# Performance work log

Hardware: AMD Instinct MI355X
Metric: run time of the kernel (lower is better)

Reference implementation:

```python
import jax, jax.numpy as jnp
import numpy as np

C = 512
B, H, W = 8, 64, 64
GROUPS = 32
EPS = 1e-6


def setup_inputs() -> dict:
    key = jax.random.key(0)
    ks = jax.random.split(key, 6)
    s = 1.0 / np.sqrt(C)
    return {
        "x": jax.random.normal(ks[0], (B, C, H, W), dtype=jnp.float32),
        "gn_scale": jnp.ones((C,), jnp.float32),
        "gn_bias": jnp.zeros((C,), jnp.float32),
        "wq": jax.random.normal(ks[1], (C, C), jnp.float32) * s,
        "bq": jnp.zeros((C,), jnp.float32),
        "wk": jax.random.normal(ks[2], (C, C), jnp.float32) * s,
        "bk": jnp.zeros((C,), jnp.float32),
        "wv": jax.random.normal(ks[3], (C, C), jnp.float32) * s,
        "bv": jnp.zeros((C,), jnp.float32),
        "wo": jax.random.normal(ks[4], (C, C), jnp.float32) * s,
        "bo": jnp.zeros((C,), jnp.float32),
    }


def group_norm(x, scale, bias):
    # x: [b, c, h, w]; GroupNorm(32 groups, eps=1e-6, affine)
    b, c, h, w = x.shape
    xg = x.reshape(b, GROUPS, c // GROUPS, h, w)
    mean = xg.mean(axis=(2, 3, 4), keepdims=True)
    var = xg.var(axis=(2, 3, 4), keepdims=True)
    xg = (xg - mean) * jax.lax.rsqrt(var + EPS)
    return xg.reshape(b, c, h, w) * scale[None, :, None, None] + bias[None, :, None, None]


def reference(x, gn_scale, gn_bias, wq, bq, wk, bk, wv, bv, wo, bo):
    b, c, h, w = x.shape
    n = h * w
    hn = group_norm(x, gn_scale, gn_bias).reshape(b, c, n)  # [b,c,n]
    # 1x1 convs == channel matmuls
    q = jnp.einsum('oc,bcn->bon', wq, hn) + bq[None, :, None]
    k = jnp.einsum('oc,bcn->bon', wk, hn) + bk[None, :, None]
    v = jnp.einsum('oc,bcn->bon', wv, hn) + bv[None, :, None]
    # scores: [b, n_query, n_key], softmax over keys
    scores = jnp.einsum('bcn,bcm->bnm', q, k) * (float(c) ** -0.5)
    attn = jax.nn.softmax(scores, axis=2)
    # out[b,c,i] = sum_j v[b,c,j] * attn[b,i,j]
    out = jnp.einsum('bcm,bnm->bcn', v, attn)
    out = jnp.einsum('oc,bcn->bon', wo, out) + bo[None, :, None]
    return x + out.reshape(b, c, h, w)
```

## Files before the change

### kernel.cpp

```cpp
#include <hip/hip_runtime.h>
#include <hip/hip_bf16.h>


typedef __bf16 bf16_t;
typedef __bf16 bf16x8 __attribute__((ext_vector_type(8)));
typedef __bf16 bf16x4 __attribute__((ext_vector_type(4)));
typedef float  f32x4  __attribute__((ext_vector_type(4)));

#define CDIM 512
#define NSP  4096
#define L2E  1.4426950408889634f

typedef __attribute__((address_space(1))) const void* as1_cvp;
typedef __attribute__((address_space(3))) void*       as3_vp;

__device__ __forceinline__ void gload_lds16(const void* g, void* l) {
  __builtin_amdgcn_global_load_lds((as1_cvp)g, (as3_vp)l, 16, 0, 0);
}

__global__ __launch_bounds__(256) void f32_to_bf16_k(const float* __restrict__ in,
                                                     bf16_t* __restrict__ out, int n) {
  int i = (blockIdx.x * 256 + threadIdx.x) * 4;
  if (i < n) {
    float4 v = *(const float4*)(in + i);
    bf16x4 o;
    o[0] = (bf16_t)v.x; o[1] = (bf16_t)v.y; o[2] = (bf16_t)v.z; o[3] = (bf16_t)v.w;
    *(bf16x4*)(out + i) = o;
  }
}

__global__ __launch_bounds__(256) void gn_stats_k(const float* __restrict__ x,
                                                  float* __restrict__ stats) {
  const int gid = blockIdx.x;
  const float4* base = (const float4*)(x + (long)gid * 65536);
  float s = 0.f, ss = 0.f;
  for (int i = threadIdx.x; i < 16384; i += 256) {
    float4 t = base[i];
    s  += t.x + t.y + t.z + t.w;
    ss += t.x*t.x + t.y*t.y + t.z*t.z + t.w*t.w;
  }
#pragma unroll
  for (int o = 32; o; o >>= 1) { s += __shfl_xor(s, o); ss += __shfl_xor(ss, o); }
  __shared__ float rs[4], rss[4];
  const int lane = threadIdx.x & 63, wid = threadIdx.x >> 6;
  if (lane == 0) { rs[wid] = s; rss[wid] = ss; }
  __syncthreads();
  if (threadIdx.x == 0) {
    s  = rs[0] + rs[1] + rs[2] + rs[3];
    ss = rss[0] + rss[1] + rss[2] + rss[3];
    float mean = s * (1.f / 65536.f);
    float var  = ss * (1.f / 65536.f) - mean * mean;
    stats[gid]       = mean;
    stats[256 + gid] = rsqrtf(var + 1e-6f);
  }
}

__global__ __launch_bounds__(256) void gn_apply_k(const float* __restrict__ x,
                                                  const float* __restrict__ stats,
                                                  const float* __restrict__ gw,
                                                  const float* __restrict__ gb,
                                                  bf16_t* __restrict__ hnT) {
  __shared__ float tile[64 * 65];
  const int n0 = blockIdx.x * 64;
  const int c0 = blockIdx.y * 64;
  const int b  = blockIdx.z;
  const int tid = threadIdx.x;
  {
    const int cl = tid >> 2, nq = tid & 3;
    const int c = c0 + cl;
    const int g = c >> 4;
    const float mean = stats[b * 32 + g];
    const float rstd = stats[256 + b * 32 + g];
    const float a  = rstd * gw[c];
    const float bb = gb[c] - mean * a;
    const float4* xr = (const float4*)(x + ((long)b * CDIM + c) * NSP + n0 + nq * 16);
#pragma unroll
    for (int i = 0; i < 4; i++) {
      float4 t = xr[i];
      float* d = &tile[cl * 65 + nq * 16 + i * 4];
      d[0] = t.x * a + bb; d[1] = t.y * a + bb; d[2] = t.z * a + bb; d[3] = t.w * a + bb;
    }
  }
  __syncthreads();
  {
    const int nl = tid >> 2, cq = tid & 3;
    union { bf16_t h[16]; uint4 v[2]; } o;
#pragma unroll
    for (int j = 0; j < 16; j++) o.h[j] = (bf16_t)tile[(cq * 16 + j) * 65 + nl];
    bf16_t* dst = hnT + ((long)b * NSP + n0 + nl) * CDIM + c0 + cq * 16;
    ((uint4*)dst)[0] = o.v[0];
    ((uint4*)dst)[1] = o.v[1];
  }
}

template <int MODE>
__global__ __launch_bounds__(256) void gemm_bt_k(
    const bf16_t* __restrict__ A, long sAb, long ldA,
    const bf16_t* __restrict__ B, long sBb, long ldB,
    void* __restrict__ Cout, long sCb, long ldC, void* __restrict__ Cout2,
    int M, int N, int K,
    const float* __restrict__ bias_row,
    const float* __restrict__ bias_col,
    float scale,
    const float* __restrict__ residual, long sRb) {
  __shared__ __align__(16) bf16_t sA[128 * 32];
  __shared__ __align__(16) bf16_t sB[128 * 32];

  const int tid  = threadIdx.x;
  const int lane = tid & 63;
  const int wid  = tid >> 6;
  const int wm = wid >> 1, wn = wid & 1;
  const int b = blockIdx.z;
  const int rowBase = blockIdx.y * 128;
  const int colBase = blockIdx.x * 128;

  const bf16_t* Ab = A + (long)b * sAb + (long)rowBase * ldA;
  const bf16_t* Bb = B + (long)b * sBb + (long)colBase * ldB;

  f32x4 acc[4][4];
#pragma unroll
  for (int i = 0; i < 4; i++)
#pragma unroll
    for (int j = 0; j < 4; j++) acc[i][j] = (f32x4){0.f, 0.f, 0.f, 0.f};

  const int q0 = tid, q1 = tid + 256;
  const int r0 = q0 >> 2, k0c = (q0 & 3) * 8;
  const int r1 = q1 >> 2, k1c = (q1 & 3) * 8;
  const int mrow  = lane & 15;
  const int kfrag = (lane >> 4) * 8;

  for (int kt = 0; kt < K; kt += 32) {
    gload_lds16(Ab + (long)r0 * ldA + kt + k0c, sA + q0 * 8);
    gload_lds16(Ab + (long)r1 * ldA + kt + k1c, sA + q1 * 8);
    gload_lds16(Bb + (long)r0 * ldB + kt + k0c, sB + q0 * 8);
    gload_lds16(Bb + (long)r1 * ldB + kt + k1c, sB + q1 * 8);
    __syncthreads();
    bf16x8 af[4], bfr[4];
#pragma unroll
    for (int t = 0; t < 4; t++) {
      af[t]  = *(const bf16x8*)&sA[(wm * 64 + t * 16 + mrow) * 32 + kfrag];
      bfr[t] = *(const bf16x8*)&sB[(wn * 64 + t * 16 + mrow) * 32 + kfrag];
    }
#pragma unroll
    for (int i = 0; i < 4; i++)
#pragma unroll
      for (int j = 0; j < 4; j++)
        acc[i][j] = __builtin_amdgcn_mfma_f32_16x16x32_bf16(af[i], bfr[j], acc[i][j], 0, 0, 0);
    __syncthreads();
  }

  const int quad = lane >> 4;
  const int colf = lane & 15;
#pragma unroll
  for (int i = 0; i < 4; i++) {
#pragma unroll
    for (int j = 0; j < 4; j++) {
#pragma unroll
      for (int r = 0; r < 4; r++) {
        const int row = rowBase + wm * 64 + i * 16 + quad * 4 + r;
        const int col = colBase + wn * 64 + j * 16 + colf;
        float v = acc[i][j][r];
        if (MODE == 2) {
          if (col < 512)
            ((bf16_t*)Cout)[(long)b * sCb + (long)row * ldC + col] =
                (bf16_t)((v + bias_col[col]) * scale);
          else
            ((bf16_t*)Cout2)[(long)b * sCb + (long)row * ldC + (col - 512)] =
                (bf16_t)(v + bias_row[col - 512]);
        } else {
          if (bias_row) v += bias_row[row];
          if (bias_col) v += bias_col[col];
          v *= scale;
          if (residual) v += residual[(long)b * sRb + (long)row * ldC + col];
          if (MODE == 1)
            ((bf16_t*)Cout)[(long)b * sCb + (long)row * ldC + col] = (bf16_t)v;
          else
            ((float*)Cout)[(long)b * sCb + (long)row * ldC + col] = v;
        }
      }
    }
  }
}

__device__ __forceinline__ void stage_k(const bf16_t* __restrict__ Kb, int j0, int h,
                                        bf16_t* dst, int tid) {
#pragma unroll
  for (int i = 0; i < 8; ++i) {
    const int e = i * 2048 + tid * 8;
    const int row = e >> 8;
    const int slot = (e >> 3) & 31;
    gload_lds16(Kb + (long)(j0 + row) * CDIM + h * 256 + ((slot ^ (row & 7)) << 3),
                dst + e);
  }
}

__device__ __forceinline__ void stage_v(const bf16_t* __restrict__ Vb, int j0, int h,
                                        bf16_t* dst, int tid) {
#pragma unroll
  for (int i = 0; i < 8; ++i) {
    const int e = i * 2048 + tid * 8;
    const int row = e >> 6;
    const int slot = (e >> 3) & 7;
    gload_lds16(Vb + (long)(h * 256 + row) * NSP + j0 + ((slot ^ (row & 7)) << 3),
                dst + e);
  }
}

#define PH_WAIT8() do { asm volatile("s_waitcnt vmcnt(8)\n\ts_barrier" ::: "memory"); \
                        __builtin_amdgcn_sched_barrier(0); } while (0)
#define PH_WAIT0() do { asm volatile("s_waitcnt vmcnt(0)\n\ts_barrier" ::: "memory"); \
                        __builtin_amdgcn_sched_barrier(0); } while (0)
#define PH_END()   do { asm volatile("s_barrier" ::: "memory"); \
                        __builtin_amdgcn_sched_barrier(0); } while (0)

__global__ __launch_bounds__(256, 2) void flash_attn_k(
    const bf16_t* __restrict__ QT, const bf16_t* __restrict__ KT,
    const bf16_t* __restrict__ V, bf16_t* __restrict__ O1T) {
  __shared__ __align__(16) bf16_t sBuf[2][16384];
  __shared__ __align__(16) bf16_t sP[4][16 * 72];

  const int tid = threadIdx.x, lane = tid & 63, w = tid >> 6;
  const int quad = lane >> 4, l15 = lane & 15;
  const int sw = l15 & 7;
  const int bid = blockIdx.x;
  const int b = bid & 7;
  const int q0 = (bid >> 3) * 64;

  const bf16_t* Qw = QT + ((long)b * NSP + q0 + w * 16) * CDIM;
  const bf16_t* Kb = KT + (long)b * NSP * CDIM;
  const bf16_t* Vb = V  + (long)b * NSP * CDIM;

  stage_k(Kb, 0, 0, &sBuf[0][0], tid);

  bf16x8 qf[16];
#pragma unroll
  for (int kc = 0; kc < 16; kc++)
    qf[kc] = *(const bf16x8*)(Qw + (long)l15 * CDIM + kc * 32 + quad * 8);

  f32x4 oacc[32];
#pragma unroll
  for (int i = 0; i < 32; i++) oacc[i] = (f32x4){0.f, 0.f, 0.f, 0.f};
  float m_r[4] = {-3e38f, -3e38f, -3e38f, -3e38f};
  float l_r[4] = {0.f, 0.f, 0.f, 0.f};

#pragma unroll 1
  for (int it = 0; it < 64; ++it) {
    const int j0 = it * 64;
    f32x4 sacc[4];
#pragma unroll
    for (int t = 0; t < 4; t++) sacc[t] = (f32x4){0.f, 0.f, 0.f, 0.f};
    bf16x8 pf0, pf1;

    stage_k(Kb, j0, 1, &sBuf[1][0], tid);
    PH_WAIT8();
    __builtin_amdgcn_s_setprio(1);
#pragma unroll
    for (int kc = 0; kc < 8; kc++) {
#pragma unroll
      for (int t = 0; t < 4; t++) {
        const bf16x8 kf = *(const bf16x8*)(
            &sBuf[0][(t * 16 + l15) * 256 + (((kc * 4 + quad) ^ sw) << 3)]);
        sacc[t] = __builtin_amdgcn_mfma_f32_16x16x32_bf16(qf[kc], kf, sacc[t], 0, 0, 0);
      }
    }
    __builtin_amdgcn_s_setprio(0);
    PH_END();

    stage_v(Vb, j0, 0, &sBuf[0][0], tid);
    PH_WAIT8();
    __builtin_amdgcn_s_setprio(1);
#pragma unroll
    for (int kc = 8; kc < 16; kc++) {
#pragma unroll
      for (int t = 0; t < 4; t++) {
        const bf16x8 kf = *(const bf16x8*)(
            &sBuf[1][(t * 16 + l15) * 256 + ((((kc - 8) * 4 + quad) ^ sw) << 3)]);
        sacc[t] = __builtin_amdgcn_mfma_f32_16x16x32_bf16(qf[kc], kf, sacc[t], 0, 0, 0);
      }
    }
    __builtin_amdgcn_s_setprio(0);

    {
      float alpha[4];
#pragma unroll
      for (int r = 0; r < 4; r++) {
        float mx = fmaxf(fmaxf(sacc[0][r], sacc[1][r]), fmaxf(sacc[2][r], sacc[3][r]));
        mx = fmaxf(mx, __shfl_xor(mx, 1));
        mx = fmaxf(mx, __shfl_xor(mx, 2));
        mx = fmaxf(mx, __shfl_xor(mx, 4));
        mx = fmaxf(mx, __shfl_xor(mx, 8));
        const float mn = fmaxf(m_r[r], mx);
        alpha[r] = exp2f((m_r[r] - mn) * L2E);
        m_r[r] = mn;
        float rs = 0.f;
#pragma unroll
        for (int t = 0; t < 4; t++) {
          const float p = exp2f((sacc[t][r] - mn) * L2E);
          sacc[t][r] = p;
          rs += p;
        }
        rs += __shfl_xor(rs, 1); rs += __shfl_xor(rs, 2);
        rs += __shfl_xor(rs, 4); rs += __shfl_xor(rs, 8);
        l_r[r] = l_r[r] * alpha[r] + rs;
      }
      const f32x4 av = {alpha[0], alpha[1], alpha[2], alpha[3]};
#pragma unroll
      for (int i = 0; i < 32; i++) oacc[i] *= av;
    }

#pragma unroll
    for (int t = 0; t < 4; t++)
#pragma unroll
      for (int r = 0; r < 4; r++)
        sP[w][(quad * 4 + r) * 72 + t * 16 + l15] = (bf16_t)sacc[t][r];
    pf0 = *(const bf16x8*)(&sP[w][l15 * 72 + quad * 8]);
    pf1 = *(const bf16x8*)(&sP[w][l15 * 72 + 32 + quad * 8]);
    PH_END();

    stage_v(Vb, j0, 1, &sBuf[1][0], tid);
    PH_WAIT8();
    __builtin_amdgcn_s_setprio(1);
#pragma unroll
    for (int ct = 0; ct < 16; ct++) {
      const int row = ct * 16 + l15;
      const bf16x8 vf0 = *(const bf16x8*)(&sBuf[0][row * 64 + ((quad ^ sw) << 3)]);
      const bf16x8 vf1 = *(const bf16x8*)(&sBuf[0][row * 64 + (((4 + quad) ^ sw) << 3)]);
      oacc[ct] = __builtin_amdgcn_mfma_f32_16x16x32_bf16(pf0, vf0, oacc[ct], 0, 0, 0);
      oacc[ct] = __builtin_amdgcn_mfma_f32_16x16x32_bf16(pf1, vf1, oacc[ct], 0, 0, 0);
    }
    __builtin_amdgcn_s_setprio(0);
    PH_END();

    if (it < 63) {
      stage_k(Kb, j0 + 64, 0, &sBuf[0][0], tid);
      PH_WAIT8();
    } else {
      PH_WAIT0();
    }
    __builtin_amdgcn_s_setprio(1);
#pragma unroll
    for (int ct = 0; ct < 16; ct++) {
      const int row = ct * 16 + l15;
      const bf16x8 vf0 = *(const bf16x8*)(&sBuf[1][row * 64 + ((quad ^ sw) << 3)]);
      const bf16x8 vf1 = *(const bf16x8*)(&sBuf[1][row * 64 + (((4 + quad) ^ sw) << 3)]);
      oacc[16 + ct] = __builtin_amdgcn_mfma_f32_16x16x32_bf16(pf0, vf0, oacc[16 + ct], 0, 0, 0);
      oacc[16 + ct] = __builtin_amdgcn_mfma_f32_16x16x32_bf16(pf1, vf1, oacc[16 + ct], 0, 0, 0);
    }
    __builtin_amdgcn_s_setprio(0);
    PH_END();
  }

  const f32x4 linv = {1.f / l_r[0], 1.f / l_r[1], 1.f / l_r[2], 1.f / l_r[3]};
  bf16_t* sO = &sBuf[0][0];
#pragma unroll
  for (int ct = 0; ct < 32; ct++) {
    const f32x4 o = oacc[ct] * linv;
#pragma unroll
    for (int r = 0; r < 4; r++)
      sO[(w * 16 + quad * 4 + r) * 512 + ct * 16 + l15] = (bf16_t)o[r];
  }
  __syncthreads();
  bf16_t* Ob = O1T + ((long)b * NSP + q0) * CDIM;
#pragma unroll
  for (int i = 0; i < 16; i++) {
    const int g = i * 256 + tid, row = g >> 6, off = g & 63;
    *(uint4*)(Ob + (long)row * CDIM + off * 8) = *(const uint4*)(sO + row * 512 + off * 8);
  }
}

extern "C" void kernel_launch(void* const* d_in, const int* in_sizes, int n_in,
                              void* d_out, int out_size, void* d_ws, size_t ws_size,
                              hipStream_t stream) {
  const float* x        = (const float*)d_in[0];
  const float* gn_scale = (const float*)d_in[1];
  const float* gn_bias  = (const float*)d_in[2];
  const float* wq = (const float*)d_in[3];
  const float* bq = (const float*)d_in[4];
  const float* wk = (const float*)d_in[5];
  const float* bk = (const float*)d_in[6];
  const float* wv = (const float*)d_in[7];
  const float* bv = (const float*)d_in[8];
  const float* wo = (const float*)d_in[9];
  const float* bo = (const float*)d_in[10];
  float* out = (float*)d_out;

  const long PB = 2097152;
  const long MB = 1048576L;
  char* w = (char*)d_ws;
  bf16_t* hnT  = (bf16_t*)(w);
  bf16_t* O1T  = hnT;
  bf16_t* QT   = (bf16_t*)(w + 32 * MB);
  bf16_t* KT   = (bf16_t*)(w + 64 * MB);
  bf16_t* V    = (bf16_t*)(w + 96 * MB);
  bf16_t* wqkb = (bf16_t*)(w + 128 * MB);
  bf16_t* wvb  = (bf16_t*)(w + 129 * MB);
  bf16_t* wob  = (bf16_t*)(w + 129 * MB + 524288L);
  float*  stats = (float*)(w + 130 * MB);

  const float qscale = 0.044194173824159216f;

  f32_to_bf16_k<<<256, 256, 0, stream>>>(wq, wqkb, 262144);
  f32_to_bf16_k<<<256, 256, 0, stream>>>(wk, wqkb + 262144, 262144);
  f32_to_bf16_k<<<256, 256, 0, stream>>>(wv, wvb, 262144);
  f32_to_bf16_k<<<256, 256, 0, stream>>>(wo, wob, 262144);

  gn_stats_k<<<256, 256, 0, stream>>>(x, stats);
  gn_apply_k<<<dim3(64, 8, 8), 256, 0, stream>>>(x, stats, gn_scale, gn_bias, hnT);

  gemm_bt_k<2><<<dim3(8, 32, 8), 256, 0, stream>>>(
      hnT, PB, 512, wqkb, 0, 512, QT, PB, 512, KT, 4096, 1024, 512,
      bk, bq, qscale, nullptr, 0);
  gemm_bt_k<1><<<dim3(32, 4, 8), 256, 0, stream>>>(
      wvb, 0, 512, hnT, PB, 512, V, PB, 4096, nullptr, 512, 4096, 512,
      bv, nullptr, 1.f, nullptr, 0);

  flash_attn_k<<<dim3(512), 256, 0, stream>>>(QT, KT, V, O1T);

  gemm_bt_k<0><<<dim3(32, 4, 8), 256, 0, stream>>>(
      wob, 0, 512, O1T, PB, 512, (void*)out, PB, 4096, nullptr, 512, 4096, 512,
      bo, nullptr, 1.f, x, PB);
}
```

Baseline: 1.141 ms.

## Double query rows per warp in flash attention, triple-buffer LDS, lazy rescale

Each wave now processes 32 query rows (two 16-row blocks) so each K/V fragment read from LDS feeds twice as many MFMAs, halving K/V traffic per query. The grid halves to 256 blocks with 128 queries each. LDS grows to three rotating buffers so K and V stages prefetch further ahead, and the online-softmax rescale of the accumulators is skipped unless the running max grows by more than a threshold. The cost is doubled accumulator registers (occupancy drops to one block per CU) and only 256 blocks, which may underfill the GPU's compute units.

```diff
diff --git a/kernel.cpp b/kernel.cpp
--- a/kernel.cpp
+++ b/kernel.cpp
@@ -206,165 +206,203 @@
   }
 }
 
-#define PH_WAIT8() do { asm volatile("s_waitcnt vmcnt(8)\n\ts_barrier" ::: "memory"); \
-                        __builtin_amdgcn_sched_barrier(0); } while (0)
-#define PH_WAIT0() do { asm volatile("s_waitcnt vmcnt(0)\n\ts_barrier" ::: "memory"); \
+#define PH_WAIT(N) do { asm volatile("s_waitcnt vmcnt(" #N ")\n\ts_barrier" ::: "memory"); \
                         __builtin_amdgcn_sched_barrier(0); } while (0)
 #define PH_END()   do { asm volatile("s_barrier" ::: "memory"); \
                         __builtin_amdgcn_sched_barrier(0); } while (0)
 
-__global__ __launch_bounds__(256, 2) void flash_attn_k(
+__global__ __launch_bounds__(256, 1) void flash_attn_k(
     const bf16_t* __restrict__ QT, const bf16_t* __restrict__ KT,
     const bf16_t* __restrict__ V, bf16_t* __restrict__ O1T) {
-  __shared__ __align__(16) bf16_t sBuf[2][16384];
-  __shared__ __align__(16) bf16_t sP[4][16 * 72];
+  __shared__ __align__(16) bf16_t sBuf[3][16384];
+  __shared__ __align__(16) bf16_t sP[4][32 * 72];
 
   const int tid = threadIdx.x, lane = tid & 63, w = tid >> 6;
   const int quad = lane >> 4, l15 = lane & 15;
   const int sw = l15 & 7;
   const int bid = blockIdx.x;
   const int b = bid & 7;
-  const int q0 = (bid >> 3) * 64;
-
-  const bf16_t* Qw = QT + ((long)b * NSP + q0 + w * 16) * CDIM;
+  const int q0 = (bid >> 3) * 128;
+
+  const bf16_t* Qw = QT + ((long)b * NSP + q0 + w * 32) * CDIM;
   const bf16_t* Kb = KT + (long)b * NSP * CDIM;
   const bf16_t* Vb = V  + (long)b * NSP * CDIM;
 
   stage_k(Kb, 0, 0, &sBuf[0][0], tid);
-
-  bf16x8 qf[16];
-#pragma unroll
-  for (int kc = 0; kc < 16; kc++)
-    qf[kc] = *(const bf16x8*)(Qw + (long)l15 * CDIM + kc * 32 + quad * 8);
-
-  f32x4 oacc[32];
-#pragma unroll
-  for (int i = 0; i < 32; i++) oacc[i] = (f32x4){0.f, 0.f, 0.f, 0.f};
-  float m_r[4] = {-3e38f, -3e38f, -3e38f, -3e38f};
-  float l_r[4] = {0.f, 0.f, 0.f, 0.f};
+  stage_k(Kb, 0, 1, &sBuf[1][0], tid);
+
+  bf16x8 qf[2][16];
+#pragma unroll
+  for (int mb = 0; mb < 2; mb++)
+#pragma unroll
+    for (int kc = 0; kc < 16; kc++)
+      qf[mb][kc] = *(const bf16x8*)(Qw + (long)(mb * 16 + l15) * CDIM + kc * 32 + quad * 8);
+
+  f32x4 oacc[2][32];
+#pragma unroll
+  for (int mb = 0; mb < 2; mb++)
+#pragma unroll
+    for (int i = 0; i < 32; i++) oacc[mb][i] = (f32x4){0.f, 0.f, 0.f, 0.f};
+  float m_r[2][4] = {{-3e38f, -3e38f, -3e38f, -3e38f}, {-3e38f, -3e38f, -3e38f, -3e38f}};
+  float l_r[2][4] = {{0.f, 0.f, 0.f, 0.f}, {0.f, 0.f, 0.f, 0.f}};
 
 #pragma unroll 1
   for (int it = 0; it < 64; ++it) {
     const int j0 = it * 64;
-    f32x4 sacc[4];
-#pragma unroll
-    for (int t = 0; t < 4; t++) sacc[t] = (f32x4){0.f, 0.f, 0.f, 0.f};
-    bf16x8 pf0, pf1;
-
-    stage_k(Kb, j0, 1, &sBuf[1][0], tid);
-    PH_WAIT8();
+    const int bA = it % 3;
+    const int bB = bA == 2 ? 0 : bA + 1;
+    const int bC = bB == 2 ? 0 : bB + 1;
+
+    f32x4 sacc[2][4];
+#pragma unroll
+    for (int mb = 0; mb < 2; mb++)
+#pragma unroll
+      for (int t = 0; t < 4; t++) sacc[mb][t] = (f32x4){0.f, 0.f, 0.f, 0.f};
+    bf16x8 pf[2][2];
+
+    stage_v(Vb, j0, 0, &sBuf[bC][0], tid);
+    PH_WAIT(16);
     __builtin_amdgcn_s_setprio(1);
 #pragma unroll
     for (int kc = 0; kc < 8; kc++) {
 #pragma unroll
       for (int t = 0; t < 4; t++) {
         const bf16x8 kf = *(const bf16x8*)(
-            &sBuf[0][(t * 16 + l15) * 256 + (((kc * 4 + quad) ^ sw) << 3)]);
-        sacc[t] = __builtin_amdgcn_mfma_f32_16x16x32_bf16(qf[kc], kf, sacc[t], 0, 0, 0);
+            &sBuf[bA][(t * 16 + l15) * 256 + (((kc * 4 + quad) ^ sw) << 3)]);
+        sacc[0][t] = __builtin_amdgcn_mfma_f32_16x16x32_bf16(qf[0][kc], kf, sacc[0][t], 0, 0, 0);
+        sacc[1][t] = __builtin_amdgcn_mfma_f32_16x16x32_bf16(qf[1][kc], kf, sacc[1][t], 0, 0, 0);
       }
     }
     __builtin_amdgcn_s_setprio(0);
     PH_END();
 
-    stage_v(Vb, j0, 0, &sBuf[0][0], tid);
-    PH_WAIT8();
+    stage_v(Vb, j0, 1, &sBuf[bA][0], tid);
+    PH_WAIT(16);
     __builtin_amdgcn_s_setprio(1);
 #pragma unroll
     for (int kc = 8; kc < 16; kc++) {
 #pragma unroll
       for (int t = 0; t < 4; t++) {
         const bf16x8 kf = *(const bf16x8*)(
-            &sBuf[1][(t * 16 + l15) * 256 + ((((kc - 8) * 4 + quad) ^ sw) << 3)]);
-        sacc[t] = __builtin_amdgcn_mfma_f32_16x16x32_bf16(qf[kc], kf, sacc[t], 0, 0, 0);
+            &sBuf[bB][(t * 16 + l15) * 256 + ((((kc - 8) * 4 + quad) ^ sw) << 3)]);
+        sacc[0][t] = __builtin_amdgcn_mfma_f32_16x16x32_bf16(qf[0][kc], kf, sacc[0][t], 0, 0, 0);
+        sacc[1][t] = __builtin_amdgcn_mfma_f32_16x16x32_bf16(qf[1][kc], kf, sacc[1][t], 0, 0, 0);
       }
     }
     __builtin_amdgcn_s_setprio(0);
 
-    {
-      float alpha[4];
+#pragma unroll
+    for (int mb = 0; mb < 2; mb++) {
+      float mx[4];
 #pragma unroll
       for (int r = 0; r < 4; r++) {
-        float mx = fmaxf(fmaxf(sacc[0][r], sacc[1][r]), fmaxf(sacc[2][r], sacc[3][r]));
-        mx = fmaxf(mx, __shfl_xor(mx, 1));
-        mx = fmaxf(mx, __shfl_xor(mx, 2));
-        mx = fmaxf(mx, __shfl_xor(mx, 4));
-        mx = fmaxf(mx, __shfl_xor(mx, 8));
-        const float mn = fmaxf(m_r[r], mx);
-        alpha[r] = exp2f((m_r[r] - mn) * L2E);
-        m_r[r] = mn;
+        float v = fmaxf(fmaxf(sacc[mb][0][r], sacc[mb][1][r]),
+                        fmaxf(sacc[mb][2][r], sacc[mb][3][r]));
+        v = fmaxf(v, __shfl_xor(v, 1));
+        v = fmaxf(v, __shfl_xor(v, 2));
+        v = fmaxf(v, __shfl_xor(v, 4));
+        v = fmaxf(v, __shfl_xor(v, 8));
+        mx[r] = v;
+      }
+      const float mg = fmaxf(fmaxf(mx[0] - m_r[mb][0], mx[1] - m_r[mb][1]),
+                             fmaxf(mx[2] - m_r[mb][2], mx[3] - m_r[mb][3]));
+      if (!__all(mg <= 8.f)) {
+        f32x4 av;
+#pragma unroll
+        for (int r = 0; r < 4; r++) {
+          const float mn = fmaxf(m_r[mb][r], mx[r]);
+          av[r] = exp2f((m_r[mb][r] - mn) * L2E);
+          m_r[mb][r] = mn;
+          l_r[mb][r] *= av[r];
+        }
+#pragma unroll
+        for (int i = 0; i < 32; i++) oacc[mb][i] *= av;
+      }
+#pragma unroll
+      for (int r = 0; r < 4; r++) {
         float rs = 0.f;
 #pragma unroll
         for (int t = 0; t < 4; t++) {
-          const float p = exp2f((sacc[t][r] - mn) * L2E);
-          sacc[t][r] = p;
+          const float p = exp2f((sacc[mb][t][r] - m_r[mb][r]) * L2E);
+          sacc[mb][t][r] = p;
           rs += p;
         }
         rs += __shfl_xor(rs, 1); rs += __shfl_xor(rs, 2);
         rs += __shfl_xor(rs, 4); rs += __shfl_xor(rs, 8);
-        l_r[r] = l_r[r] * alpha[r] + rs;
-      }
-      const f32x4 av = {alpha[0], alpha[1], alpha[2], alpha[3]};
-#pragma unroll
-      for (int i = 0; i < 32; i++) oacc[i] *= av;
-    }
-
-#pragma unroll
-    for (int t = 0; t < 4; t++)
-#pragma unroll
-      for (int r = 0; r < 4; r++)
-        sP[w][(quad * 4 + r) * 72 + t * 16 + l15] = (bf16_t)sacc[t][r];
-    pf0 = *(const bf16x8*)(&sP[w][l15 * 72 + quad * 8]);
-    pf1 = *(const bf16x8*)(&sP[w][l15 * 72 + 32 + quad * 8]);
+        l_r[mb][r] += rs;
+      }
+#pragma unroll
+      for (int t = 0; t < 4; t++)
+#pragma unroll
+        for (int r = 0; r < 4; r++)
+          sP[w][(mb * 16 + quad * 4 + r) * 72 + t * 16 + l15] = (bf16_t)sacc[mb][t][r];
+      pf[mb][0] = *(const bf16x8*)(&sP[w][(mb * 16 + l15) * 72 + quad * 8]);
+      pf[mb][1] = *(const bf16x8*)(&sP[w][(mb * 16 + l15) * 72 + 32 + quad * 8]);
+    }
     PH_END();
 
-    stage_v(Vb, j0, 1, &sBuf[1][0], tid);
-    PH_WAIT8();
+    if (it < 63) {
+      stage_k(Kb, j0 + 64, 0, &sBuf[bB][0], tid);
+      PH_WAIT(16);
+    } else {
+      PH_WAIT(8);
+    }
     __builtin_amdgcn_s_setprio(1);
 #pragma unroll
     for (int ct = 0; ct < 16; ct++) {
       const int row = ct * 16 + l15;
-      const bf16x8 vf0 = *(const bf16x8*)(&sBuf[0][row * 64 + ((quad ^ sw) << 3)]);
-      const bf16x8 vf1 = *(const bf16x8*)(&sBuf[0][row * 64 + (((4 + quad) ^ sw) << 3)]);
-      oacc[ct] = __builtin_amdgcn_mfma_f32_16x16x32_bf16(pf0, vf0, oacc[ct], 0, 0, 0);
-      oacc[ct] = __builtin_amdgcn_mfma_f32_16x16x32_bf16(pf1, vf1, oacc[ct], 0, 0, 0);
+      const bf16x8 vf0 = *(const bf16x8*)(&sBuf[bC][row * 64 + ((quad ^ sw) << 3)]);
+      const bf16x8 vf1 = *(const bf16x8*)(&sBuf[bC][row * 64 + (((4 + quad) ^ sw) << 3)]);
+      oacc[0][ct] = __builtin_amdgcn_mfma_f32_16x16x32_bf16(pf[0][0], vf0, oacc[0][ct], 0, 0, 0);
+      oacc[0][ct] = __builtin_amdgcn_mfma_f32_16x16x32_bf16(pf[0][1], vf1, oacc[0][ct], 0, 0, 0);
+      oacc[1][ct] = __builtin_amdgcn_mfma_f32_16x16x32_bf16(pf[1][0], vf0, oacc[1][ct], 0, 0, 0);
+      oacc[1][ct] = __builtin_amdgcn_mfma_f32_16x16x32_bf16(pf[1][1], vf1, oacc[1][ct], 0, 0, 0);
     }
     __builtin_amdgcn_s_setprio(0);
     PH_END();
 
     if (it < 63) {
-      stage_k(Kb, j0 + 64, 0, &sBuf[0][0], tid);
-      PH_WAIT8();
+      stage_k(Kb, j0 + 64, 1, &sBuf[bC][0], tid);
+      PH_WAIT(16);
     } else {
-      PH_WAIT0();
+      PH_WAIT(0);
     }
     __builtin_amdgcn_s_setprio(1);
 #pragma unroll
     for (int ct = 0; ct < 16; ct++) {
       const int row = ct * 16 + l15;
-      const bf16x8 vf0 = *(const bf16x8*)(&sBuf[1][row * 64 + ((quad ^ sw) << 3)]);
-      const bf16x8 vf1 = *(const bf16x8*)(&sBuf[1][row * 64 + (((4 + quad) ^ sw) << 3)]);
-      oacc[16 + ct] = __builtin_amdgcn_mfma_f32_16x16x32_bf16(pf0, vf0, oacc[16 + ct], 0, 0, 0);
-      oacc[16 + ct] = __builtin_amdgcn_mfma_f32_16x16x32_bf16(pf1, vf1, oacc[16 + ct], 0, 0, 0);
+      const bf16x8 vf0 = *(const bf16x8*)(&sBuf[bA][row * 64 + ((quad ^ sw) << 3)]);
+      const bf16x8 vf1 = *(const bf16x8*)(&sBuf[bA][row * 64 + (((4 + quad) ^ sw) << 3)]);
+      oacc[0][16 + ct] = __builtin_amdgcn_mfma_f32_16x16x32_bf16(pf[0][0], vf0, oacc[0][16 + ct], 0, 0, 0);
+      oacc[0][16 + ct] = __builtin_amdgcn_mfma_f32_16x16x32_bf16(pf[0][1], vf1, oacc[0][16 + ct], 0, 0, 0);
+      oacc[1][16 + ct] = __builtin_amdgcn_mfma_f32_16x16x32_bf16(pf[1][0], vf0, oacc[1][16 + ct], 0, 0, 0);
+      oacc[1][16 + ct] = __builtin_amdgcn_mfma_f32_16x16x32_bf16(pf[1][1], vf1, oacc[1][16 + ct], 0, 0, 0);
     }
     __builtin_amdgcn_s_setprio(0);
     PH_END();
   }
 
-  const f32x4 linv = {1.f / l_r[0], 1.f / l_r[1], 1.f / l_r[2], 1.f / l_r[3]};
   bf16_t* sO = &sBuf[0][0];
-#pragma unroll
-  for (int ct = 0; ct < 32; ct++) {
-    const f32x4 o = oacc[ct] * linv;
-#pragma unroll
-    for (int r = 0; r < 4; r++)
-      sO[(w * 16 + quad * 4 + r) * 512 + ct * 16 + l15] = (bf16_t)o[r];
-  }
-  __syncthreads();
   bf16_t* Ob = O1T + ((long)b * NSP + q0) * CDIM;
 #pragma unroll
-  for (int i = 0; i < 16; i++) {
-    const int g = i * 256 + tid, row = g >> 6, off = g & 63;
-    *(uint4*)(Ob + (long)row * CDIM + off * 8) = *(const uint4*)(sO + row * 512 + off * 8);
+  for (int mb = 0; mb < 2; mb++) {
+    const f32x4 linv = {1.f / l_r[mb][0], 1.f / l_r[mb][1],
+                        1.f / l_r[mb][2], 1.f / l_r[mb][3]};
+    __syncthreads();
+#pragma unroll
+    for (int ct = 0; ct < 32; ct++) {
+      const f32x4 o = oacc[mb][ct] * linv;
+#pragma unroll
+      for (int r = 0; r < 4; r++)
+        sO[(w * 16 + quad * 4 + r) * 520 + ct * 16 + l15] = (bf16_t)o[r];
+    }
+    __syncthreads();
+#pragma unroll
+    for (int i = 0; i < 16; i++) {
+      const int g = i * 256 + tid, row = g >> 6, off = g & 63;
+      const int dr = (row >> 4) * 32 + mb * 16 + (row & 15);
+      *(uint4*)(Ob + (long)dr * CDIM + off * 8) = *(const uint4*)(sO + row * 520 + off * 8);
+    }
   }
 }
 
@@ -414,7 +452,7 @@
       wvb, 0, 512, hnT, PB, 512, V, PB, 4096, nullptr, 512, 4096, 512,
       bv, nullptr, 1.f, nullptr, 0);
 
-  flash_attn_k<<<dim3(512), 256, 0, stream>>>(QT, KT, V, O1T);
+  flash_attn_k<<<dim3(256), 256, 0, stream>>>(QT, KT, V, O1T);
 
   gemm_bt_k<0><<<dim3(32, 4, 8), 256, 0, stream>>>(
       wob, 0, 512, O1T, PB, 512, (void*)out, PB, 4096, nullptr, 512, 4096, 512,
```

Result: slower. 2.098 ms (+83.8%).

## Split PV matmul by channel slices per wave, sharing P across waves

Applied to the files above, without the earlier changes.

The P·V stage is repartitioned so each wave computes all 64 query rows for its own 64-channel slice. Each wave loads only its own V slice and reads every wave's P tile from shared memory, with per-row rescale factors and final normalizers passed through a new shared alpha buffer. This removes the block-wide barrier wait on V loads (per-wave vmcnt only) and cuts redundant V fragment reads per wave by reusing each V fragment across four P tiles. The grid is also reordered so batch is blockIdx.y and query tiles vary fastest, which changes which blocks share K/V in cache. Cost: extra shared-memory traffic for P and alpha, plus more sync dependencies.

```diff
diff --git a/kernel.cpp b/kernel.cpp
--- a/kernel.cpp
+++ b/kernel.cpp
@@ -194,37 +194,37 @@
   }
 }
 
-__device__ __forceinline__ void stage_v(const bf16_t* __restrict__ Vb, int j0, int h,
-                                        bf16_t* dst, int tid) {
+__device__ __forceinline__ void stage_v_slice(const bf16_t* __restrict__ Vb, int j0,
+                                              int h, bf16_t* slab, int w, int lane) {
 #pragma unroll
   for (int i = 0; i < 8; ++i) {
-    const int e = i * 2048 + tid * 8;
-    const int row = e >> 6;
+    const int e = i * 512 + lane * 8;
+    const int cc = e >> 6;
     const int slot = (e >> 3) & 7;
-    gload_lds16(Vb + (long)(h * 256 + row) * NSP + j0 + ((slot ^ (row & 7)) << 3),
-                dst + e);
-  }
-}
-
-#define PH_WAIT8() do { asm volatile("s_waitcnt vmcnt(8)\n\ts_barrier" ::: "memory"); \
-                        __builtin_amdgcn_sched_barrier(0); } while (0)
-#define PH_WAIT0() do { asm volatile("s_waitcnt vmcnt(0)\n\ts_barrier" ::: "memory"); \
-                        __builtin_amdgcn_sched_barrier(0); } while (0)
-#define PH_END()   do { asm volatile("s_barrier" ::: "memory"); \
-                        __builtin_amdgcn_sched_barrier(0); } while (0)
+    gload_lds16(Vb + (long)(h * 256 + w * 64 + cc) * NSP + j0 + ((slot ^ (cc & 7)) << 3),
+                slab + e);
+  }
+}
+
+#define PH_WAITB(N) do { asm volatile("s_waitcnt vmcnt(" #N ")\n\ts_barrier" ::: "memory"); \
+                         __builtin_amdgcn_sched_barrier(0); } while (0)
+#define PH_VM(N)    do { asm volatile("s_waitcnt vmcnt(" #N ")" ::: "memory"); \
+                         __builtin_amdgcn_sched_barrier(0); } while (0)
+#define PH_END()    do { asm volatile("s_barrier" ::: "memory"); \
+                         __builtin_amdgcn_sched_barrier(0); } while (0)
 
 __global__ __launch_bounds__(256, 2) void flash_attn_k(
     const bf16_t* __restrict__ QT, const bf16_t* __restrict__ KT,
     const bf16_t* __restrict__ V, bf16_t* __restrict__ O1T) {
   __shared__ __align__(16) bf16_t sBuf[2][16384];
   __shared__ __align__(16) bf16_t sP[4][16 * 72];
+  __shared__ __align__(16) float  sAlpha[64];
 
   const int tid = threadIdx.x, lane = tid & 63, w = tid >> 6;
   const int quad = lane >> 4, l15 = lane & 15;
   const int sw = l15 & 7;
-  const int bid = blockIdx.x;
-  const int b = bid & 7;
-  const int q0 = (bid >> 3) * 64;
+  const int b  = blockIdx.y;
+  const int q0 = blockIdx.x * 64;
 
   const bf16_t* Qw = QT + ((long)b * NSP + q0 + w * 16) * CDIM;
   const bf16_t* Kb = KT + (long)b * NSP * CDIM;
@@ -237,9 +237,11 @@
   for (int kc = 0; kc < 16; kc++)
     qf[kc] = *(const bf16x8*)(Qw + (long)l15 * CDIM + kc * 32 + quad * 8);
 
-  f32x4 oacc[32];
-#pragma unroll
-  for (int i = 0; i < 32; i++) oacc[i] = (f32x4){0.f, 0.f, 0.f, 0.f};
+  f32x4 oacc[4][8];
+#pragma unroll
+  for (int t = 0; t < 4; t++)
+#pragma unroll
+    for (int j = 0; j < 8; j++) oacc[t][j] = (f32x4){0.f, 0.f, 0.f, 0.f};
   float m_r[4] = {-3e38f, -3e38f, -3e38f, -3e38f};
   float l_r[4] = {0.f, 0.f, 0.f, 0.f};
 
@@ -249,10 +251,9 @@
     f32x4 sacc[4];
 #pragma unroll
     for (int t = 0; t < 4; t++) sacc[t] = (f32x4){0.f, 0.f, 0.f, 0.f};
-    bf16x8 pf0, pf1;
 
     stage_k(Kb, j0, 1, &sBuf[1][0], tid);
-    PH_WAIT8();
+    PH_WAITB(8);
     __builtin_amdgcn_s_setprio(1);
 #pragma unroll
     for (int kc = 0; kc < 8; kc++) {
@@ -266,8 +267,8 @@
     __builtin_amdgcn_s_setprio(0);
     PH_END();
 
-    stage_v(Vb, j0, 0, &sBuf[0][0], tid);
-    PH_WAIT8();
+    stage_v_slice(Vb, j0, 0, &sBuf[0][w * 4096], w, lane);
+    PH_WAITB(8);
     __builtin_amdgcn_s_setprio(1);
 #pragma unroll
     for (int kc = 8; kc < 16; kc++) {
@@ -302,62 +303,91 @@
         rs += __shfl_xor(rs, 1); rs += __shfl_xor(rs, 2);
         rs += __shfl_xor(rs, 4); rs += __shfl_xor(rs, 8);
         l_r[r] = l_r[r] * alpha[r] + rs;
-      }
-      const f32x4 av = {alpha[0], alpha[1], alpha[2], alpha[3]};
-#pragma unroll
-      for (int i = 0; i < 32; i++) oacc[i] *= av;
-    }
-
-#pragma unroll
-    for (int t = 0; t < 4; t++)
-#pragma unroll
-      for (int r = 0; r < 4; r++)
-        sP[w][(quad * 4 + r) * 72 + t * 16 + l15] = (bf16_t)sacc[t][r];
-    pf0 = *(const bf16x8*)(&sP[w][l15 * 72 + quad * 8]);
-    pf1 = *(const bf16x8*)(&sP[w][l15 * 72 + 32 + quad * 8]);
+        if (l15 == 0) sAlpha[w * 16 + quad * 4 + r] = alpha[r];
+      }
+#pragma unroll
+      for (int t = 0; t < 4; t++)
+#pragma unroll
+        for (int r = 0; r < 4; r++)
+          sP[w][(quad * 4 + r) * 72 + t * 16 + l15] = (bf16_t)sacc[t][r];
+    }
     PH_END();
 
-    stage_v(Vb, j0, 1, &sBuf[1][0], tid);
-    PH_WAIT8();
+    stage_v_slice(Vb, j0, 1, &sBuf[1][w * 4096], w, lane);
+    PH_VM(8);
+    {
+#pragma unroll
+      for (int t = 0; t < 4; t++) {
+        const f32x4 av = *(const f32x4*)(&sAlpha[t * 16 + quad * 4]);
+#pragma unroll
+        for (int j = 0; j < 8; j++) oacc[t][j] *= av;
+      }
+    }
     __builtin_amdgcn_s_setprio(1);
 #pragma unroll
-    for (int ct = 0; ct < 16; ct++) {
-      const int row = ct * 16 + l15;
-      const bf16x8 vf0 = *(const bf16x8*)(&sBuf[0][row * 64 + ((quad ^ sw) << 3)]);
-      const bf16x8 vf1 = *(const bf16x8*)(&sBuf[0][row * 64 + (((4 + quad) ^ sw) << 3)]);
-      oacc[ct] = __builtin_amdgcn_mfma_f32_16x16x32_bf16(pf0, vf0, oacc[ct], 0, 0, 0);
-      oacc[ct] = __builtin_amdgcn_mfma_f32_16x16x32_bf16(pf1, vf1, oacc[ct], 0, 0, 0);
+    for (int kc2 = 0; kc2 < 2; kc2++) {
+      bf16x8 pf[4];
+#pragma unroll
+      for (int t = 0; t < 4; t++)
+        pf[t] = *(const bf16x8*)(&sP[t][l15 * 72 + kc2 * 32 + quad * 8]);
+#pragma unroll
+      for (int j = 0; j < 4; j++) {
+        const int rr = j * 16 + l15;
+        const bf16x8 vf = *(const bf16x8*)(
+            &sBuf[0][w * 4096 + rr * 64 + (((kc2 * 4 + quad) ^ sw) << 3)]);
+#pragma unroll
+        for (int t = 0; t < 4; t++)
+          oacc[t][j] = __builtin_amdgcn_mfma_f32_16x16x32_bf16(pf[t], vf, oacc[t][j], 0, 0, 0);
+      }
     }
     __builtin_amdgcn_s_setprio(0);
     PH_END();
 
     if (it < 63) {
       stage_k(Kb, j0 + 64, 0, &sBuf[0][0], tid);
-      PH_WAIT8();
+      PH_VM(8);
     } else {
-      PH_WAIT0();
+      PH_VM(0);
     }
     __builtin_amdgcn_s_setprio(1);
 #pragma unroll
-    for (int ct = 0; ct < 16; ct++) {
-      const int row = ct * 16 + l15;
-      const bf16x8 vf0 = *(const bf16x8*)(&sBuf[1][row * 64 + ((quad ^ sw) << 3)]);
-      const bf16x8 vf1 = *(const bf16x8*)(&sBuf[1][row * 64 + (((4 + quad) ^ sw) << 3)]);
-      oacc[16 + ct] = __builtin_amdgcn_mfma_f32_16x16x32_bf16(pf0, vf0, oacc[16 + ct], 0, 0, 0);
-      oacc[16 + ct] = __builtin_amdgcn_mfma_f32_16x16x32_bf16(pf1, vf1, oacc[16 + ct], 0, 0, 0);
+    for (int kc2 = 0; kc2 < 2; kc2++) {
+      bf16x8 pf[4];
+#pragma unroll
+      for (int t = 0; t < 4; t++)
+        pf[t] = *(const bf16x8*)(&sP[t][l15 * 72 + kc2 * 32 + quad * 8]);
+#pragma unroll
+      for (int j = 0; j < 4; j++) {
+        const int rr = j * 16 + l15;
+        const bf16x8 vf = *(const bf16x8*)(
+            &sBuf[1][w * 4096 + rr * 64 + (((kc2 * 4 + quad) ^ sw) << 3)]);
+#pragma unroll
+        for (int t = 0; t < 4; t++)
+          oacc[t][4 + j] = __builtin_amdgcn_mfma_f32_16x16x32_bf16(pf[t], vf, oacc[t][4 + j], 0, 0, 0);
+      }
     }
     __builtin_amdgcn_s_setprio(0);
     PH_END();
   }
 
-  const f32x4 linv = {1.f / l_r[0], 1.f / l_r[1], 1.f / l_r[2], 1.f / l_r[3]};
+  if (l15 == 0) {
+#pragma unroll
+    for (int r = 0; r < 4; r++) sAlpha[w * 16 + quad * 4 + r] = l_r[r];
+  }
+  __syncthreads();
   bf16_t* sO = &sBuf[0][0];
 #pragma unroll
-  for (int ct = 0; ct < 32; ct++) {
-    const f32x4 o = oacc[ct] * linv;
-#pragma unroll
-    for (int r = 0; r < 4; r++)
-      sO[(w * 16 + quad * 4 + r) * 512 + ct * 16 + l15] = (bf16_t)o[r];
+  for (int t = 0; t < 4; t++) {
+    const f32x4 lv = *(const f32x4*)(&sAlpha[t * 16 + quad * 4]);
+    const f32x4 linv = {1.f / lv[0], 1.f / lv[1], 1.f / lv[2], 1.f / lv[3]};
+#pragma unroll
+    for (int j = 0; j < 8; j++) {
+      const int ch = (j < 4 ? w * 64 + j * 16 : 256 + w * 64 + (j - 4) * 16) + l15;
+      const f32x4 o = oacc[t][j] * linv;
+#pragma unroll
+      for (int r = 0; r < 4; r++)
+        sO[(t * 16 + quad * 4 + r) * 512 + ch] = (bf16_t)o[r];
+    }
   }
   __syncthreads();
   bf16_t* Ob = O1T + ((long)b * NSP + q0) * CDIM;
@@ -414,7 +444,7 @@
       wvb, 0, 512, hnT, PB, 512, V, PB, 4096, nullptr, 512, 4096, 512,
       bv, nullptr, 1.f, nullptr, 0);
 
-  flash_attn_k<<<dim3(512), 256, 0, stream>>>(QT, KT, V, O1T);
+  flash_attn_k<<<dim3(64, 8), 256, 0, stream>>>(QT, KT, V, O1T);
 
   gemm_bt_k<0><<<dim3(32, 4, 8), 256, 0, stream>>>(
       wob, 0, 512, O1T, PB, 512, (void*)out, PB, 4096, nullptr, 512, 4096, 512,
```

Result: slower. 1.832 ms (+60.6%).

## Lazy softmax rescaling, MFMA row-sum, and batch-major attention grid

Applied to the files above, without the earlier changes.

The online softmax in the attention kernel now rescales the output accumulators only when some row's running max grows by more than a threshold anywhere in the wavefront, which removes the 32-accumulator multiply on most iterations. The row-sum shuffles are replaced by two MFMAs against a ones vector, reusing the bf16 P fragments. The grid becomes 2D with the batch on the y axis, so adjacent blocks share the same K/V batch and get better L2 locality. The risks are that the row sum now uses bf16-rounded probabilities, and that with a stale max the exponentials can grow up to about e^8, which slightly changes numerics.

```diff
diff --git a/kernel.cpp b/kernel.cpp
--- a/kernel.cpp
+++ b/kernel.cpp
@@ -222,9 +222,8 @@
   const int tid = threadIdx.x, lane = tid & 63, w = tid >> 6;
   const int quad = lane >> 4, l15 = lane & 15;
   const int sw = l15 & 7;
-  const int bid = blockIdx.x;
-  const int b = bid & 7;
-  const int q0 = (bid >> 3) * 64;
+  const int b  = blockIdx.y;
+  const int q0 = blockIdx.x * 64;
 
   const bf16_t* Qw = QT + ((long)b * NSP + q0 + w * 16) * CDIM;
   const bf16_t* Kb = KT + (long)b * NSP * CDIM;
@@ -237,11 +236,15 @@
   for (int kc = 0; kc < 16; kc++)
     qf[kc] = *(const bf16x8*)(Qw + (long)l15 * CDIM + kc * 32 + quad * 8);
 
+  bf16x8 vone;
+#pragma unroll
+  for (int j = 0; j < 8; j++) vone[j] = (bf16_t)1.0f;
+
   f32x4 oacc[32];
 #pragma unroll
   for (int i = 0; i < 32; i++) oacc[i] = (f32x4){0.f, 0.f, 0.f, 0.f};
   float m_r[4] = {-3e38f, -3e38f, -3e38f, -3e38f};
-  float l_r[4] = {0.f, 0.f, 0.f, 0.f};
+  f32x4 lacc = (f32x4){0.f, 0.f, 0.f, 0.f};
 
 #pragma unroll 1
   for (int it = 0; it < 64; ++it) {
@@ -281,40 +284,41 @@
     __builtin_amdgcn_s_setprio(0);
 
     {
-      float alpha[4];
+      float mx[4];
 #pragma unroll
       for (int r = 0; r < 4; r++) {
-        float mx = fmaxf(fmaxf(sacc[0][r], sacc[1][r]), fmaxf(sacc[2][r], sacc[3][r]));
-        mx = fmaxf(mx, __shfl_xor(mx, 1));
-        mx = fmaxf(mx, __shfl_xor(mx, 2));
-        mx = fmaxf(mx, __shfl_xor(mx, 4));
-        mx = fmaxf(mx, __shfl_xor(mx, 8));
-        const float mn = fmaxf(m_r[r], mx);
-        alpha[r] = exp2f((m_r[r] - mn) * L2E);
-        m_r[r] = mn;
-        float rs = 0.f;
-#pragma unroll
-        for (int t = 0; t < 4; t++) {
-          const float p = exp2f((sacc[t][r] - mn) * L2E);
-          sacc[t][r] = p;
-          rs += p;
+        float v = fmaxf(fmaxf(sacc[0][r], sacc[1][r]), fmaxf(sacc[2][r], sacc[3][r]));
+        v = fmaxf(v, __shfl_xor(v, 1));
+        v = fmaxf(v, __shfl_xor(v, 2));
+        v = fmaxf(v, __shfl_xor(v, 4));
+        v = fmaxf(v, __shfl_xor(v, 8));
+        mx[r] = v;
+      }
+      const float growth = fmaxf(fmaxf(mx[0] - m_r[0], mx[1] - m_r[1]),
+                                 fmaxf(mx[2] - m_r[2], mx[3] - m_r[3]));
+      if (!__all(growth <= 8.f)) {
+        f32x4 av;
+#pragma unroll
+        for (int r = 0; r < 4; r++) {
+          const float mn = fmaxf(m_r[r], mx[r]);
+          av[r] = exp2f((m_r[r] - mn) * L2E);
+          m_r[r] = mn;
         }
-        rs += __shfl_xor(rs, 1); rs += __shfl_xor(rs, 2);
-        rs += __shfl_xor(rs, 4); rs += __shfl_xor(rs, 8);
-        l_r[r] = l_r[r] * alpha[r] + rs;
+#pragma unroll
+        for (int i = 0; i < 32; i++) oacc[i] *= av;
+        lacc *= av;
       }
-      const f32x4 av = {alpha[0], alpha[1], alpha[2], alpha[3]};
-#pragma unroll
-      for (int i = 0; i < 32; i++) oacc[i] *= av;
-    }
-
-#pragma unroll
-    for (int t = 0; t < 4; t++)
-#pragma unroll
-      for (int r = 0; r < 4; r++)
-        sP[w][(quad * 4 + r) * 72 + t * 16 + l15] = (bf16_t)sacc[t][r];
+#pragma unroll
+      for (int t = 0; t < 4; t++)
+#pragma unroll
+        for (int r = 0; r < 4; r++)
+          sP[w][(quad * 4 + r) * 72 + t * 16 + l15] =
+              (bf16_t)exp2f((sacc[t][r] - m_r[r]) * L2E);
+    }
     pf0 = *(const bf16x8*)(&sP[w][l15 * 72 + quad * 8]);
     pf1 = *(const bf16x8*)(&sP[w][l15 * 72 + 32 + quad * 8]);
+    lacc = __builtin_amdgcn_mfma_f32_16x16x32_bf16(pf0, vone, lacc, 0, 0, 0);
+    lacc = __builtin_amdgcn_mfma_f32_16x16x32_bf16(pf1, vone, lacc, 0, 0, 0);
     PH_END();
 
     stage_v(Vb, j0, 1, &sBuf[1][0], tid);
@@ -350,7 +354,7 @@
     PH_END();
   }
 
-  const f32x4 linv = {1.f / l_r[0], 1.f / l_r[1], 1.f / l_r[2], 1.f / l_r[3]};
+  const f32x4 linv = {1.f / lacc[0], 1.f / lacc[1], 1.f / lacc[2], 1.f / lacc[3]};
   bf16_t* sO = &sBuf[0][0];
 #pragma unroll
   for (int ct = 0; ct < 32; ct++) {
@@ -414,7 +418,7 @@
       wvb, 0, 512, hnT, PB, 512, V, PB, 4096, nullptr, 512, 4096, 512,
       bv, nullptr, 1.f, nullptr, 0);
 
-  flash_attn_k<<<dim3(512), 256, 0, stream>>>(QT, KT, V, O1T);
+  flash_attn_k<<<dim3(64, 8), 256, 0, stream>>>(QT, KT, V, O1T);
 
   gemm_bt_k<0><<<dim3(32, 4, 8), 256, 0, stream>>>(
       wob, 0, 512, O1T, PB, 512, (void*)out, PB, 4096, nullptr, 512, 4096, 512,
```

Result: slower. 1.389 ms (+21.7%).
